# Kernel tuning notes

Measured on AMD Instinct MI355X. Metric: run time of the kernel, lower is better.

The kernel has to match this reference:

```python
import jax, jax.numpy as jnp
import numpy as np

N_HEAD = 4
N_FEAT = 256
D_K = N_FEAT // N_HEAD
MAX_SEQ_LEN = 500
LN_EPS = 1e-6


def setup_inputs() -> dict:
    key = jax.random.key(0)
    ks = jax.random.split(key, 12)
    B, L, F = 64, 500, N_FEAT
    s = lambda fan_in: 1.0 / np.sqrt(fan_in)
    return {
        "q": jax.random.normal(ks[0], (B, L, F), jnp.float32),
        "k": jax.random.normal(ks[1], (B, L, F), jnp.float32),
        "v": jax.random.normal(ks[2], (B, L, F), jnp.float32),
        # weights stored as [in, out] (torch Linear transposed)
        "w_qs": jax.random.normal(ks[3], (F, F), jnp.float32) * s(F),
        "w_vs": jax.random.normal(ks[4], (F, F), jnp.float32) * s(F),
        "w1": jax.random.normal(ks[5], (D_K, D_K), jnp.float32) * s(D_K),
        "b1": jax.random.normal(ks[6], (D_K,), jnp.float32) * s(D_K),
        "w2": jax.random.normal(ks[7], (D_K, MAX_SEQ_LEN), jnp.float32) * s(D_K),
        "b2": jax.random.normal(ks[8], (MAX_SEQ_LEN,), jnp.float32) * s(D_K),
        "fc_w": jax.random.normal(ks[9], (F, F), jnp.float32) * s(F),
        "ln_g": jnp.ones((F,), jnp.float32),
        "ln_b": jnp.zeros((F,), jnp.float32),
    }


def reference(q, k, v, w_qs, w_vs, w1, b1, w2, b2, fc_w, ln_g, ln_b):
    B, L, F = q.shape
    H, dk = N_HEAD, D_K
    residual = q
    # head projections -> [B, H, L, dk]
    qh = (q @ w_qs).reshape(B, L, H, dk).transpose(0, 2, 1, 3)
    vh = (v @ w_vs).reshape(B, L, H, dk).transpose(0, 2, 1, 3)
    # dense synthesizer: relu(q W1 + b1) W2 + b2, slice to len_q
    weight = jax.nn.relu(qh @ w1 + b1)
    attn = (weight @ w2 + b2)[..., :L]            # [B, H, L, L]
    attn = jax.nn.softmax(attn, axis=-1)
    out = attn @ vh                                # [B, H, L, dk]
    out = out.transpose(0, 2, 1, 3).reshape(B, L, F)
    out = out @ fc_w + residual
    # LayerNorm(eps=1e-6)
    mu = jnp.mean(out, axis=-1, keepdims=True)
    var = jnp.var(out, axis=-1, keepdims=True)
    out = (out - mu) * jax.lax.rsqrt(var + LN_EPS) * ln_g + ln_b
    return out
```

## Files before the change

### kernel.cpp

```cpp
#include <hip/hip_runtime.h>
#include <math.h>

#define B_   64
#define L_   500
#define F_   256
#define H_   4
#define DK   64
#define LOG2E 1.44269504088896340736f

typedef unsigned short u16;
typedef unsigned int   u32;
typedef __attribute__((ext_vector_type(8))) short short8;
typedef __attribute__((ext_vector_type(4))) float f32x4;

static __device__ __forceinline__ u16 f2bf(float f) {
    u32 u = __float_as_uint(f);
    u32 r = (u + 0x7FFFu + ((u >> 16) & 1u)) >> 16;
    return (u16)r;
}
static __device__ __forceinline__ u32 pk_bf16_up(float x, float y) {
    u32 xb = __float_as_uint(x) + 0x8000u;
    u32 yb = __float_as_uint(y) + 0x8000u;
    return (xb >> 16) | (yb & 0xFFFF0000u);
}
static __device__ __forceinline__ float exp2_fast(float x) {
#if __has_builtin(__builtin_amdgcn_exp2f)
    return __builtin_amdgcn_exp2f(x);
#else
    return exp2f(x);
#endif
}

typedef __attribute__((address_space(3))) u32 lds32;
typedef const __attribute__((address_space(1))) u32 gbl32;
static __device__ __forceinline__ void gload_lds16(const u16* g, u16* l) {
    __builtin_amdgcn_global_load_lds((gbl32*)g, (lds32*)l, 16, 0, 0);
}

__global__ __launch_bounds__(256) void prep_kernel(
    const float* __restrict__ wq, const float* __restrict__ wv,
    const float* __restrict__ fcw, const float* __restrict__ w1,
    const float* __restrict__ w2, const float* __restrict__ b2,
    u16* __restrict__ wqT, u16* __restrict__ wvT, u16* __restrict__ fcwT,
    u16* __restrict__ w1T, u16* __restrict__ w2sw,
    u16* __restrict__ qh_bf, u16* __restrict__ vhT, float* __restrict__ b2p)
{
    int t = blockIdx.x * 256 + threadIdx.x;
    int stride = gridDim.x * 256;
    for (int i = t; i < 256 * 256; i += stride) {
        int n = i >> 8, k = i & 255;
        wqT[i]  = f2bf(wq[k * 256 + n]);
        wvT[i]  = f2bf(wv[k * 256 + n]);
        fcwT[i] = f2bf(fcw[k * 256 + n]);
    }
    for (int i = t; i < 64 * 64; i += stride) {
        int n = i >> 6, k = i & 63;
        w1T[i] = f2bf(w1[k * 64 + n]);
    }
    for (int i = t; i < 512 * 64; i += stride) {
        int cc  = i >> 12;
        int row = (i >> 6) & 63;
        int kc  = i & 63;
        int n   = cc * 64 + row;
        int kl  = kc ^ ((row & 7) << 3);
        w2sw[i] = f2bf((n < 500 ? w2[kl * 500 + n] : 0.f) * LOG2E);
    }
    for (int i = t; i < 512; i += stride)
        b2p[i] = (i < 500) ? b2[i] * LOG2E : -1e30f;
    for (int i = t; i < 3072; i += stride)
        qh_bf[8192000 + i] = 0;
    for (int i = t; i < 196608; i += stride) {
        int bh = i / 768;
        int r  = i - bh * 768;
        int d  = r / 12;
        int kk = 52 + (r - d * 12);
        vhT[((size_t)((bh * 8 + 7) * 64 + d)) * 64 + (kk ^ ((d & 7) << 3))] = 0;
    }
}

__global__ __launch_bounds__(512) void proj_kernel(
    const float* __restrict__ q, const float* __restrict__ v,
    const u16* __restrict__ wqT, const u16* __restrict__ wvT,
    u16* __restrict__ qh_bf, u16* __restrict__ vhT)
{
    const int which = blockIdx.y;
    const float* __restrict__ x = which ? v : q;
    const u16*   __restrict__ wT = which ? wvT : wqT;

    __shared__ u16 Xs[64][72];
    __shared__ u16 Ws[256][72];

    const int tid  = threadIdx.x;
    const int wvid = tid >> 6, ln = tid & 63;
    const int n16  = ln & 15, quad = ln >> 4;
    const int wr   = wvid >> 2, wc = wvid & 3;
    const int row0 = blockIdx.x * 64;

    f32x4 acc[2][4];
    #pragma unroll
    for (int mt = 0; mt < 2; mt++)
        #pragma unroll
        for (int nt = 0; nt < 4; nt++) acc[mt][nt] = (f32x4){0.f, 0.f, 0.f, 0.f};

    for (int kc = 0; kc < 256; kc += 64) {
        #pragma unroll
        for (int j = 0; j < 2; j++) {
            int idx = tid + 512 * j;
            int m = idx >> 4, k4 = idx & 15;
            float4 a = *(const float4*)&x[(size_t)(row0 + m) * 256 + kc + k4 * 4];
            __align__(8) u16 t4[4] = {f2bf(a.x), f2bf(a.y), f2bf(a.z), f2bf(a.w)};
            *(uint2*)&Xs[m][k4 * 4] = *(const uint2*)t4;
        }
        #pragma unroll
        for (int j = 0; j < 4; j++) {
            int idx = tid + 512 * j;
            int n = idx >> 3, k8 = idx & 7;
            *(uint4*)&Ws[n][k8 * 8] = *(const uint4*)&wT[n * 256 + kc + k8 * 8];
        }
        __syncthreads();
        #pragma unroll
        for (int ks = 0; ks < 2; ks++) {
            short8 af[2], bfr[4];
            #pragma unroll
            for (int mt = 0; mt < 2; mt++)
                af[mt] = *(const short8*)&Xs[wr * 32 + mt * 16 + n16][ks * 32 + quad * 8];
            #pragma unroll
            for (int nt = 0; nt < 4; nt++)
                bfr[nt] = *(const short8*)&Ws[wc * 64 + nt * 16 + n16][ks * 32 + quad * 8];
            #pragma unroll
            for (int mt = 0; mt < 2; mt++)
                #pragma unroll
                for (int nt = 0; nt < 4; nt++)
                    acc[mt][nt] = __builtin_amdgcn_mfma_f32_16x16x32_bf16(
                        af[mt], bfr[nt], acc[mt][nt], 0, 0, 0);
        }
        __syncthreads();
    }

    if (which == 0) {
        #pragma unroll
        for (int mt = 0; mt < 2; mt++) {
            int m0 = row0 + wr * 32 + mt * 16 + quad * 4;
            int b  = m0 / 500;
            int l0 = m0 - 500 * b;
            #pragma unroll
            for (int nt = 0; nt < 4; nt++) {
                int d = nt * 16 + n16;
                u16* dst = qh_bf + ((size_t)((b * 4 + wc) * 500 + l0)) * 64 + d;
                #pragma unroll
                for (int i = 0; i < 4; i++)
                    dst[(size_t)i * 64] = f2bf(acc[mt][nt][i]);
            }
        }
    } else {
        #pragma unroll
        for (int mt = 0; mt < 2; mt++) {
            int m0 = row0 + wr * 32 + mt * 16 + quad * 4;
            int b  = m0 / 500;
            int l0 = m0 - 500 * b;
            int cc = l0 >> 6, kk = l0 & 63;
            #pragma unroll
            for (int nt = 0; nt < 4; nt++) {
                int d = nt * 16 + n16;
                __align__(8) u16 t4[4];
                #pragma unroll
                for (int i = 0; i < 4; i++) t4[i] = f2bf(acc[mt][nt][i]);
                size_t base = ((size_t)(((b * 4 + wc) * 8 + cc) * 64 + d)) * 64;
                *(uint2*)&vhT[base + (kk ^ ((d & 7) << 3))] = *(const uint2*)t4;
            }
        }
    }
}

__global__ __launch_bounds__(512, 1) void attn_kernel(
    const u16* __restrict__ qh, const u16* __restrict__ vhT,
    const u16* __restrict__ w1T, const float* __restrict__ b1,
    const u16* __restrict__ w2sw, const float* __restrict__ b2p,
    u16* __restrict__ ctx)
{
    __shared__ __align__(16) u16 w2all[32768];
    __shared__ __align__(16) u16 v_s[2][4096];
    __shared__ __align__(16) float b2s[512];
    __shared__ __align__(16) u16 scr[8][4][16][72];

    const int tid  = threadIdx.x;
    const int wv   = tid >> 6;
    const int ln   = tid & 63;
    const int n16  = ln & 15;
    const int quad = ln >> 4;
    const int bh   = blockIdx.x;
    const int r0   = wv * 64;

    const u16* vg = vhT + (size_t)bh * 32768;

    {
        int base = wv * 4096;
        #pragma unroll
        for (int j = 0; j < 8; j++)
            gload_lds16(w2sw + base + j * 512 + ln * 8, &w2all[base + j * 512]);
        gload_lds16(vg + wv * 512 + ln * 8, &v_s[0][wv * 512]);
        if (wv < 2)
            gload_lds16((const u16*)b2p + wv * 512 + ln * 8, (u16*)&b2s[wv * 256]);
    }

    const int b = bh >> 2, h = bh & 3;

    {
        short8 a0[4], a1[4];
        #pragma unroll
        for (int rg = 0; rg < 4; rg++) {
            const u16* qbase =
                qh + ((size_t)(bh * 500 + r0 + rg * 16 + n16)) * 64;
            a0[rg] = *(const short8*)(qbase + quad * 8);
            a1[rg] = *(const short8*)(qbase + 32 + quad * 8);
        }
        #pragma unroll
        for (int nt = 0; nt < 4; nt++) {
            const u16* wb = w1T + (nt * 16 + n16) * 64;
            short8 wA0 = *(const short8*)(wb + quad * 8);
            short8 wA1 = *(const short8*)(wb + 32 + quad * 8);
            float4 bv = *(const float4*)&b1[nt * 16 + quad * 4];
            #pragma unroll
            for (int rg = 0; rg < 4; rg++) {
                f32x4 c = {bv.x, bv.y, bv.z, bv.w};
                c = __builtin_amdgcn_mfma_f32_16x16x32_bf16(wA0, a0[rg], c, 0, 0, 0);
                c = __builtin_amdgcn_mfma_f32_16x16x32_bf16(wA1, a1[rg], c, 0, 0, 0);
                u32 p01 = pk_bf16_up(fmaxf(c[0], 0.f), fmaxf(c[1], 0.f));
                u32 p23 = pk_bf16_up(fmaxf(c[2], 0.f), fmaxf(c[3], 0.f));
                *(uint2*)&scr[wv][rg][n16][nt * 16 + quad * 4] =
                    make_uint2(p01, p23);
            }
        }
    }
    short8 sa0[4], sa1[4];
    #pragma unroll
    for (int rg = 0; rg < 4; rg++) {
        sa0[rg] = *(const short8*)&scr[wv][rg][n16][quad * 8];
        sa1[rg] = *(const short8*)&scr[wv][rg][n16][32 + quad * 8];
    }

    f32x4 oacc[4][4];
    #pragma unroll
    for (int rg = 0; rg < 4; rg++)
        #pragma unroll
        for (int nt = 0; nt < 4; nt++)
            oacc[rg][nt] = (f32x4){0.f, 0.f, 0.f, 0.f};
    float sm[4] = {0.f, 0.f, 0.f, 0.f};

    __syncthreads();

    #pragma unroll 2
    for (int cc = 0; cc < 8; cc++) {
        if (cc < 7)
            gload_lds16(vg + (cc + 1) * 4096 + wv * 512 + ln * 8,
                        &v_s[(cc + 1) & 1][wv * 512]);
        const u16* vbuf = &v_s[cc & 1][0];

        #pragma unroll
        for (int t = 0; t < 4; t++) {
            int r  = t * 16 + n16;
            int sw = (r & 7) << 3;
            const u16* wb = &w2all[cc * 4096 + r * 64];
            short8 wA0 = *(const short8*)&wb[(quad * 8) ^ sw];
            short8 wA1 = *(const short8*)&wb[(32 + quad * 8) ^ sw];
            float4 bv = *(const float4*)&b2s[cc * 64 + t * 16 + quad * 4];
            #pragma unroll
            for (int rg = 0; rg < 4; rg++) {
                f32x4 c = {bv.x, bv.y, bv.z, bv.w};
                c = __builtin_amdgcn_mfma_f32_16x16x32_bf16(wA0, sa0[rg], c, 0, 0, 0);
                c = __builtin_amdgcn_mfma_f32_16x16x32_bf16(wA1, sa1[rg], c, 0, 0, 0);
                float e0 = exp2_fast(c[0]);
                float e1 = exp2_fast(c[1]);
                float e2 = exp2_fast(c[2]);
                float e3 = exp2_fast(c[3]);
                sm[rg] += (e0 + e1) + (e2 + e3);
                *(uint2*)&scr[wv][rg][n16][t * 16 + quad * 4] =
                    make_uint2(pk_bf16_up(e0, e1), pk_bf16_up(e2, e3));
            }
        }
        #pragma unroll
        for (int ks = 0; ks < 2; ks++) {
            short8 pa[4];
            #pragma unroll
            for (int rg = 0; rg < 4; rg++)
                pa[rg] = *(const short8*)&scr[wv][rg][n16][ks * 32 + quad * 8];
            #pragma unroll
            for (int nt = 0; nt < 4; nt++) {
                int d   = nt * 16 + n16;
                int swd = (d & 7) << 3;
                short8 vb = *(const short8*)&vbuf[d * 64 +
                                                  ((ks * 32 + quad * 8) ^ swd)];
                #pragma unroll
                for (int rg = 0; rg < 4; rg++)
                    oacc[rg][nt] = __builtin_amdgcn_mfma_f32_16x16x32_bf16(
                        pa[rg], vb, oacc[rg][nt], 0, 0, 0);
            }
        }
        __syncthreads();
    }

    #pragma unroll
    for (int rg = 0; rg < 4; rg++) {
        float smt = sm[rg];
        smt += __shfl_xor(smt, 16);
        smt += __shfl_xor(smt, 32);
        #pragma unroll
        for (int i = 0; i < 4; i++) {
            int lrow = r0 + rg * 16 + quad * 4 + i;
            float si = __shfl(smt, quad * 4 + i);
            if (lrow < 500) {
                float s = 1.f / si;
                u16* dst = &ctx[((size_t)(b * 500 + lrow)) * 256 + h * 64];
                #pragma unroll
                for (int nt = 0; nt < 4; nt++)
                    dst[nt * 16 + n16] = f2bf(oacc[rg][nt][i] * s);
            }
        }
    }
}

__global__ __launch_bounds__(512) void final_kernel(
    const u16* __restrict__ ctx, const u16* __restrict__ fcwT,
    const float* __restrict__ qres, const float* __restrict__ g,
    const float* __restrict__ bta, float* __restrict__ out)
{
    __shared__ u16 Xs[64][72];
    __shared__ u16 Ws[256][72];
    __shared__ float red[4][2][64];
    __shared__ float murs[2][64];

    const int tid  = threadIdx.x;
    const int wvid = tid >> 6, ln = tid & 63;
    const int n16  = ln & 15, quad = ln >> 4;
    const int wr   = wvid >> 2, wc = wvid & 3;
    const int row0 = blockIdx.x * 64;

    f32x4 acc[2][4];
    #pragma unroll
    for (int mt = 0; mt < 2; mt++)
        #pragma unroll
        for (int nt = 0; nt < 4; nt++) acc[mt][nt] = (f32x4){0.f, 0.f, 0.f, 0.f};

    for (int kc = 0; kc < 256; kc += 64) {
        {
            int idx = tid;
            int m = idx >> 3, k8 = idx & 7;
            *(uint4*)&Xs[m][k8 * 8] =
                *(const uint4*)&ctx[(size_t)(row0 + m) * 256 + kc + k8 * 8];
        }
        #pragma unroll
        for (int j = 0; j < 4; j++) {
            int idx = tid + 512 * j;
            int n = idx >> 3, k8 = idx & 7;
            *(uint4*)&Ws[n][k8 * 8] = *(const uint4*)&fcwT[n * 256 + kc + k8 * 8];
        }
        __syncthreads();
        #pragma unroll
        for (int ks = 0; ks < 2; ks++) {
            short8 af[2], bfr[4];
            #pragma unroll
            for (int mt = 0; mt < 2; mt++)
                af[mt] = *(const short8*)&Xs[wr * 32 + mt * 16 + n16][ks * 32 + quad * 8];
            #pragma unroll
            for (int nt = 0; nt < 4; nt++)
                bfr[nt] = *(const short8*)&Ws[wc * 64 + nt * 16 + n16][ks * 32 + quad * 8];
            #pragma unroll
            for (int mt = 0; mt < 2; mt++)
                #pragma unroll
                for (int nt = 0; nt < 4; nt++)
                    acc[mt][nt] = __builtin_amdgcn_mfma_f32_16x16x32_bf16(
                        af[mt], bfr[nt], acc[mt][nt], 0, 0, 0);
        }
        __syncthreads();
    }

    #pragma unroll
    for (int mt = 0; mt < 2; mt++) {
        int m0 = row0 + wr * 32 + mt * 16 + quad * 4;
        #pragma unroll
        for (int i = 0; i < 4; i++) {
            const float* rp = &qres[(size_t)(m0 + i) * 256 + wc * 64 + n16];
            #pragma unroll
            for (int nt = 0; nt < 4; nt++)
                acc[mt][nt][i] += rp[nt * 16];
        }
    }
    #pragma unroll
    for (int mt = 0; mt < 2; mt++) {
        #pragma unroll
        for (int i = 0; i < 4; i++) {
            float s1 = 0.f, s2 = 0.f;
            #pragma unroll
            for (int nt = 0; nt < 4; nt++) {
                float vv = acc[mt][nt][i];
                s1 += vv; s2 += vv * vv;
            }
            #pragma unroll
            for (int off = 1; off < 16; off <<= 1) {
                s1 += __shfl_xor(s1, off);
                s2 += __shfl_xor(s2, off);
            }
            if (n16 == 0) {
                int r = wr * 32 + mt * 16 + quad * 4 + i;
                red[wc][0][r] = s1;
                red[wc][1][r] = s2;
            }
        }
    }
    __syncthreads();
    if (tid < 64) {
        float S1 = red[0][0][tid] + red[1][0][tid] + red[2][0][tid] + red[3][0][tid];
        float S2 = red[0][1][tid] + red[1][1][tid] + red[2][1][tid] + red[3][1][tid];
        float mu  = S1 * 0.00390625f;
        float var = S2 * 0.00390625f - mu * mu;
        murs[0][tid] = mu;
        murs[1][tid] = rsqrtf(var + 1e-6f);
    }
    __syncthreads();

    float gv[4], bv[4];
    #pragma unroll
    for (int nt = 0; nt < 4; nt++) {
        int col = wc * 64 + nt * 16 + n16;
        gv[nt] = g[col];
        bv[nt] = bta[col];
    }
    #pragma unroll
    for (int mt = 0; mt < 2; mt++) {
        int rb = wr * 32 + mt * 16 + quad * 4;
        #pragma unroll
        for (int i = 0; i < 4; i++) {
            float mu = murs[0][rb + i];
            float rs = murs[1][rb + i];
            float* op = &out[(size_t)(row0 + rb + i) * 256 + wc * 64 + n16];
            #pragma unroll
            for (int nt = 0; nt < 4; nt++)
                op[nt * 16] = (acc[mt][nt][i] - mu) * rs * gv[nt] + bv[nt];
        }
    }
}

extern "C" void kernel_launch(void* const* d_in, const int* in_sizes, int n_in,
                              void* d_out, int out_size, void* d_ws, size_t ws_size,
                              hipStream_t stream)
{
    const float* q   = (const float*)d_in[0];
    const float* v   = (const float*)d_in[2];
    const float* wqs = (const float*)d_in[3];
    const float* wvs = (const float*)d_in[4];
    const float* w1  = (const float*)d_in[5];
    const float* b1  = (const float*)d_in[6];
    const float* w2  = (const float*)d_in[7];
    const float* b2  = (const float*)d_in[8];
    const float* fcw = (const float*)d_in[9];
    const float* lng = (const float*)d_in[10];
    const float* lnb = (const float*)d_in[11];
    float* out = (float*)d_out;

    u16* qh_bf = (u16*)d_ws;
    u16* vhT   = qh_bf + 8200192;
    u16* w1T   = vhT + 8388608;
    u16* w2sw  = w1T + 4096;
    u16* wqT   = w2sw + 32768;
    u16* wvT   = wqT + 65536;
    u16* fcwT  = wvT + 65536;
    u16* ctx   = fcwT + 65536;
    float* b2p = (float*)(qh_bf + 8195072);

    prep_kernel <<<dim3(64),     256, 0, stream>>>(wqs, wvs, fcw, w1, w2, b2,
                                                   wqT, wvT, fcwT, w1T, w2sw,
                                                   qh_bf, vhT, b2p);
    proj_kernel <<<dim3(500, 2), 512, 0, stream>>>(q, v, wqT, wvT, qh_bf, vhT);
    attn_kernel <<<dim3(256),    512, 0, stream>>>(qh_bf, vhT, w1T, b1, w2sw, b2p, ctx);
    final_kernel<<<dim3(500),    512, 0, stream>>>(ctx, fcwT, q, lng, lnb, out);
}
```

Baseline: 83.58 us.

## Restructure projection GEMM with 128-row tiles, swizzled LDS and async double-buffered weights

After: 89.60 us. +7.2%, slower.

```diff
diff --git a/kernel.cpp b/kernel.cpp
--- a/kernel.cpp
+++ b/kernel.cpp
@@ -41,7 +41,7 @@
     const float* __restrict__ wq, const float* __restrict__ wv,
     const float* __restrict__ fcw, const float* __restrict__ w1,
     const float* __restrict__ w2, const float* __restrict__ b2,
-    u16* __restrict__ wqT, u16* __restrict__ wvT, u16* __restrict__ fcwT,
+    u16* __restrict__ wqsw, u16* __restrict__ wvsw, u16* __restrict__ fcwT,
     u16* __restrict__ w1T, u16* __restrict__ w2sw,
     u16* __restrict__ qh_bf, u16* __restrict__ vhT, float* __restrict__ b2p)
 {
@@ -49,9 +49,15 @@
     int stride = gridDim.x * 256;
     for (int i = t; i < 256 * 256; i += stride) {
         int n = i >> 8, k = i & 255;
-        wqT[i]  = f2bf(wq[k * 256 + n]);
-        wvT[i]  = f2bf(wv[k * 256 + n]);
         fcwT[i] = f2bf(fcw[k * 256 + n]);
+    }
+    for (int i = t; i < 256 * 256; i += stride) {
+        int kc = i >> 14;
+        int n  = (i >> 6) & 255;
+        int k  = i & 63;
+        int kl = kc * 64 + (k ^ ((n & 7) << 3));
+        wqsw[i] = f2bf(wq[kl * 256 + n]);
+        wvsw[i] = f2bf(wv[kl * 256 + n]);
     }
     for (int i = t; i < 64 * 64; i += stride) {
         int n = i >> 6, k = i & 63;
@@ -78,57 +84,78 @@
     }
 }
 
-__global__ __launch_bounds__(512) void proj_kernel(
+__global__ __launch_bounds__(512, 1) void proj_kernel(
     const float* __restrict__ q, const float* __restrict__ v,
-    const u16* __restrict__ wqT, const u16* __restrict__ wvT,
+    const u16* __restrict__ wqsw, const u16* __restrict__ wvsw,
     u16* __restrict__ qh_bf, u16* __restrict__ vhT)
 {
     const int which = blockIdx.y;
     const float* __restrict__ x = which ? v : q;
-    const u16*   __restrict__ wT = which ? wvT : wqT;
-
-    __shared__ u16 Xs[64][72];
-    __shared__ u16 Ws[256][72];
+    const u16*   __restrict__ wsw = which ? wvsw : wqsw;
+
+    __shared__ __align__(16) u16 Xs[128 * 256];
+    __shared__ __align__(16) u16 Ws[2][16384];
 
     const int tid  = threadIdx.x;
     const int wvid = tid >> 6, ln = tid & 63;
     const int n16  = ln & 15, quad = ln >> 4;
     const int wr   = wvid >> 2, wc = wvid & 3;
-    const int row0 = blockIdx.x * 64;
-
-    f32x4 acc[2][4];
-    #pragma unroll
-    for (int mt = 0; mt < 2; mt++)
+    const int row0 = blockIdx.x * 128;
+
+    float4 xv[16];
+    #pragma unroll
+    for (int j = 0; j < 16; j++) {
+        int idx = tid + 512 * j;
+        int m = idx >> 6, k4 = idx & 63;
+        xv[j] = *(const float4*)&x[(size_t)(row0 + m) * 256 + k4 * 4];
+    }
+    #pragma unroll
+    for (int j = 0; j < 4; j++)
+        gload_lds16(wsw + wvid * 2048 + j * 512 + ln * 8,
+                    &Ws[0][wvid * 2048 + j * 512]);
+    #pragma unroll
+    for (int j = 0; j < 16; j++) {
+        int idx = tid + 512 * j;
+        int m = idx >> 6, k = (idx & 63) * 4;
+        int kx = k ^ ((m & 7) << 3);
+        *(uint2*)&Xs[m * 256 + kx] =
+            make_uint2(pk_bf16_up(xv[j].x, xv[j].y), pk_bf16_up(xv[j].z, xv[j].w));
+    }
+
+    f32x4 acc[4][4];
+    #pragma unroll
+    for (int mt = 0; mt < 4; mt++)
         #pragma unroll
         for (int nt = 0; nt < 4; nt++) acc[mt][nt] = (f32x4){0.f, 0.f, 0.f, 0.f};
 
-    for (int kc = 0; kc < 256; kc += 64) {
-        #pragma unroll
-        for (int j = 0; j < 2; j++) {
-            int idx = tid + 512 * j;
-            int m = idx >> 4, k4 = idx & 15;
-            float4 a = *(const float4*)&x[(size_t)(row0 + m) * 256 + kc + k4 * 4];
-            __align__(8) u16 t4[4] = {f2bf(a.x), f2bf(a.y), f2bf(a.z), f2bf(a.w)};
-            *(uint2*)&Xs[m][k4 * 4] = *(const uint2*)t4;
-        }
-        #pragma unroll
-        for (int j = 0; j < 4; j++) {
-            int idx = tid + 512 * j;
-            int n = idx >> 3, k8 = idx & 7;
-            *(uint4*)&Ws[n][k8 * 8] = *(const uint4*)&wT[n * 256 + kc + k8 * 8];
-        }
-        __syncthreads();
+    __syncthreads();
+
+    #pragma unroll 2
+    for (int cc = 0; cc < 4; cc++) {
+        if (cc < 3) {
+            #pragma unroll
+            for (int j = 0; j < 4; j++)
+                gload_lds16(wsw + (cc + 1) * 16384 + wvid * 2048 + j * 512 + ln * 8,
+                            &Ws[(cc + 1) & 1][wvid * 2048 + j * 512]);
+        }
+        const u16* wb = &Ws[cc & 1][0];
         #pragma unroll
         for (int ks = 0; ks < 2; ks++) {
-            short8 af[2], bfr[4];
-            #pragma unroll
-            for (int mt = 0; mt < 2; mt++)
-                af[mt] = *(const short8*)&Xs[wr * 32 + mt * 16 + n16][ks * 32 + quad * 8];
-            #pragma unroll
-            for (int nt = 0; nt < 4; nt++)
-                bfr[nt] = *(const short8*)&Ws[wc * 64 + nt * 16 + n16][ks * 32 + quad * 8];
-            #pragma unroll
-            for (int mt = 0; mt < 2; mt++)
+            short8 af[4], bfr[4];
+            #pragma unroll
+            for (int mt = 0; mt < 4; mt++) {
+                int m = wr * 64 + mt * 16 + n16;
+                int k = cc * 64 + ks * 32 + quad * 8;
+                af[mt] = *(const short8*)&Xs[m * 256 + (k ^ ((m & 7) << 3))];
+            }
+            #pragma unroll
+            for (int nt = 0; nt < 4; nt++) {
+                int r = wc * 64 + nt * 16 + n16;
+                bfr[nt] = *(const short8*)&wb[r * 64 +
+                                              ((ks * 32 + quad * 8) ^ ((r & 7) << 3))];
+            }
+            #pragma unroll
+            for (int mt = 0; mt < 4; mt++)
                 #pragma unroll
                 for (int nt = 0; nt < 4; nt++)
                     acc[mt][nt] = __builtin_amdgcn_mfma_f32_16x16x32_bf16(
@@ -139,8 +166,8 @@
 
     if (which == 0) {
         #pragma unroll
-        for (int mt = 0; mt < 2; mt++) {
-            int m0 = row0 + wr * 32 + mt * 16 + quad * 4;
+        for (int mt = 0; mt < 4; mt++) {
+            int m0 = row0 + wr * 64 + mt * 16 + quad * 4;
             int b  = m0 / 500;
             int l0 = m0 - 500 * b;
             #pragma unroll
@@ -154,18 +181,18 @@
         }
     } else {
         #pragma unroll
-        for (int mt = 0; mt < 2; mt++) {
-            int m0 = row0 + wr * 32 + mt * 16 + quad * 4;
+        for (int mt = 0; mt < 4; mt++) {
+            int m0 = row0 + wr * 64 + mt * 16 + quad * 4;
             int b  = m0 / 500;
             int l0 = m0 - 500 * b;
-            int cc = l0 >> 6, kk = l0 & 63;
+            int vc = l0 >> 6, kk = l0 & 63;
             #pragma unroll
             for (int nt = 0; nt < 4; nt++) {
                 int d = nt * 16 + n16;
                 __align__(8) u16 t4[4];
                 #pragma unroll
                 for (int i = 0; i < 4; i++) t4[i] = f2bf(acc[mt][nt][i]);
-                size_t base = ((size_t)(((b * 4 + wc) * 8 + cc) * 64 + d)) * 64;
+                size_t base = ((size_t)(((b * 4 + wc) * 8 + vc) * 64 + d)) * 64;
                 *(uint2*)&vhT[base + (kk ^ ((d & 7) << 3))] = *(const uint2*)t4;
             }
         }
@@ -461,16 +488,16 @@
     u16* vhT   = qh_bf + 8200192;
     u16* w1T   = vhT + 8388608;
     u16* w2sw  = w1T + 4096;
-    u16* wqT   = w2sw + 32768;
-    u16* wvT   = wqT + 65536;
-    u16* fcwT  = wvT + 65536;
+    u16* wqsw  = w2sw + 32768;
+    u16* wvsw  = wqsw + 65536;
+    u16* fcwT  = wvsw + 65536;
     u16* ctx   = fcwT + 65536;
     float* b2p = (float*)(qh_bf + 8195072);
 
     prep_kernel <<<dim3(64),     256, 0, stream>>>(wqs, wvs, fcw, w1, w2, b2,
-                                                   wqT, wvT, fcwT, w1T, w2sw,
+                                                   wqsw, wvsw, fcwT, w1T, w2sw,
                                                    qh_bf, vhT, b2p);
-    proj_kernel <<<dim3(500, 2), 512, 0, stream>>>(q, v, wqT, wvT, qh_bf, vhT);
+    proj_kernel <<<dim3(250, 2), 512, 0, stream>>>(q, v, wqsw, wvsw, qh_bf, vhT);
     attn_kernel <<<dim3(256),    512, 0, stream>>>(qh_bf, vhT, w1T, b1, w2sw, b2p, ctx);
     final_kernel<<<dim3(500),    512, 0, stream>>>(ctx, fcwT, q, lng, lnb, out);
 }
```

## Pre-swizzle projection weights into MFMA fragment order and double-buffer input tile

Applied to the files above, without the earlier changes.

New measurement: 85.24 us. No clear change (+2.0%).

```diff
diff --git a/kernel.cpp b/kernel.cpp
--- a/kernel.cpp
+++ b/kernel.cpp
@@ -41,7 +41,7 @@
     const float* __restrict__ wq, const float* __restrict__ wv,
     const float* __restrict__ fcw, const float* __restrict__ w1,
     const float* __restrict__ w2, const float* __restrict__ b2,
-    u16* __restrict__ wqT, u16* __restrict__ wvT, u16* __restrict__ fcwT,
+    u16* __restrict__ wqf, u16* __restrict__ wvf, u16* __restrict__ fcwT,
     u16* __restrict__ w1T, u16* __restrict__ w2sw,
     u16* __restrict__ qh_bf, u16* __restrict__ vhT, float* __restrict__ b2p)
 {
@@ -49,9 +49,18 @@
     int stride = gridDim.x * 256;
     for (int i = t; i < 256 * 256; i += stride) {
         int n = i >> 8, k = i & 255;
-        wqT[i]  = f2bf(wq[k * 256 + n]);
-        wvT[i]  = f2bf(wv[k * 256 + n]);
         fcwT[i] = f2bf(fcw[k * 256 + n]);
+    }
+    for (int i = t; i < 65536; i += stride) {
+        int j  = i & 7;
+        int ln = (i >> 3) & 63;
+        int tn = (i >> 9) & 15;
+        int ks = (i >> 13) & 1;
+        int kc = i >> 14;
+        int k  = kc * 64 + ks * 32 + (ln >> 4) * 8 + j;
+        int n  = tn * 16 + (ln & 15);
+        wqf[i] = f2bf(wq[k * 256 + n]);
+        wvf[i] = f2bf(wv[k * 256 + n]);
     }
     for (int i = t; i < 64 * 64; i += stride) {
         int n = i >> 6, k = i & 63;
@@ -80,15 +89,14 @@
 
 __global__ __launch_bounds__(512) void proj_kernel(
     const float* __restrict__ q, const float* __restrict__ v,
-    const u16* __restrict__ wqT, const u16* __restrict__ wvT,
+    const u16* __restrict__ wqf, const u16* __restrict__ wvf,
     u16* __restrict__ qh_bf, u16* __restrict__ vhT)
 {
     const int which = blockIdx.y;
     const float* __restrict__ x = which ? v : q;
-    const u16*   __restrict__ wT = which ? wvT : wqT;
-
-    __shared__ u16 Xs[64][72];
-    __shared__ u16 Ws[256][72];
+    const u16*   __restrict__ wf = which ? wvf : wqf;
+
+    __shared__ __align__(16) u16 Xs[2][64][72];
 
     const int tid  = threadIdx.x;
     const int wvid = tid >> 6, ln = tid & 63;
@@ -102,37 +110,47 @@
         #pragma unroll
         for (int nt = 0; nt < 4; nt++) acc[mt][nt] = (f32x4){0.f, 0.f, 0.f, 0.f};
 
-    for (int kc = 0; kc < 256; kc += 64) {
-        #pragma unroll
-        for (int j = 0; j < 2; j++) {
-            int idx = tid + 512 * j;
-            int m = idx >> 4, k4 = idx & 15;
-            float4 a = *(const float4*)&x[(size_t)(row0 + m) * 256 + kc + k4 * 4];
-            __align__(8) u16 t4[4] = {f2bf(a.x), f2bf(a.y), f2bf(a.z), f2bf(a.w)};
-            *(uint2*)&Xs[m][k4 * 4] = *(const uint2*)t4;
-        }
-        #pragma unroll
-        for (int j = 0; j < 4; j++) {
-            int idx = tid + 512 * j;
-            int n = idx >> 3, k8 = idx & 7;
-            *(uint4*)&Ws[n][k8 * 8] = *(const uint4*)&wT[n * 256 + kc + k8 * 8];
-        }
-        __syncthreads();
+    #pragma unroll
+    for (int j = 0; j < 2; j++) {
+        int idx = tid + 512 * j;
+        int m = idx >> 4, k4 = idx & 15;
+        float4 a = *(const float4*)&x[(size_t)(row0 + m) * 256 + k4 * 4];
+        *(uint2*)&Xs[0][m][k4 * 4] =
+            make_uint2(pk_bf16_up(a.x, a.y), pk_bf16_up(a.z, a.w));
+    }
+    __syncthreads();
+
+    #pragma unroll
+    for (int kc = 0; kc < 4; kc++) {
+        const int cur = kc & 1;
+        if (kc < 3) {
+            #pragma unroll
+            for (int j = 0; j < 2; j++) {
+                int idx = tid + 512 * j;
+                int m = idx >> 4, k4 = idx & 15;
+                float4 a = *(const float4*)&x[(size_t)(row0 + m) * 256 +
+                                              (kc + 1) * 64 + k4 * 4];
+                *(uint2*)&Xs[cur ^ 1][m][k4 * 4] =
+                    make_uint2(pk_bf16_up(a.x, a.y), pk_bf16_up(a.z, a.w));
+            }
+        }
         #pragma unroll
         for (int ks = 0; ks < 2; ks++) {
-            short8 af[2], bfr[4];
+            short8 af[2];
             #pragma unroll
             for (int mt = 0; mt < 2; mt++)
-                af[mt] = *(const short8*)&Xs[wr * 32 + mt * 16 + n16][ks * 32 + quad * 8];
-            #pragma unroll
-            for (int nt = 0; nt < 4; nt++)
-                bfr[nt] = *(const short8*)&Ws[wc * 64 + nt * 16 + n16][ks * 32 + quad * 8];
-            #pragma unroll
-            for (int mt = 0; mt < 2; mt++)
-                #pragma unroll
-                for (int nt = 0; nt < 4; nt++)
+                af[mt] = *(const short8*)&Xs[cur][wr * 32 + mt * 16 + n16]
+                                            [ks * 32 + quad * 8];
+            #pragma unroll
+            for (int nt = 0; nt < 4; nt++) {
+                const u16* fp = wf + ((((kc * 2 + ks) * 16) + (wc * 4 + nt)) * 64
+                                      + ln) * 8;
+                short8 bfr = *(const short8*)fp;
+                #pragma unroll
+                for (int mt = 0; mt < 2; mt++)
                     acc[mt][nt] = __builtin_amdgcn_mfma_f32_16x16x32_bf16(
-                        af[mt], bfr[nt], acc[mt][nt], 0, 0, 0);
+                        af[mt], bfr, acc[mt][nt], 0, 0, 0);
+            }
         }
         __syncthreads();
     }
@@ -158,15 +176,15 @@
             int m0 = row0 + wr * 32 + mt * 16 + quad * 4;
             int b  = m0 / 500;
             int l0 = m0 - 500 * b;
-            int cc = l0 >> 6, kk = l0 & 63;
+            int vc = l0 >> 6, kk2 = l0 & 63;
             #pragma unroll
             for (int nt = 0; nt < 4; nt++) {
                 int d = nt * 16 + n16;
                 __align__(8) u16 t4[4];
                 #pragma unroll
                 for (int i = 0; i < 4; i++) t4[i] = f2bf(acc[mt][nt][i]);
-                size_t base = ((size_t)(((b * 4 + wc) * 8 + cc) * 64 + d)) * 64;
-                *(uint2*)&vhT[base + (kk ^ ((d & 7) << 3))] = *(const uint2*)t4;
+                size_t base = ((size_t)(((b * 4 + wc) * 8 + vc) * 64 + d)) * 64;
+                *(uint2*)&vhT[base + (kk2 ^ ((d & 7) << 3))] = *(const uint2*)t4;
             }
         }
     }
@@ -461,16 +479,16 @@
     u16* vhT   = qh_bf + 8200192;
     u16* w1T   = vhT + 8388608;
     u16* w2sw  = w1T + 4096;
-    u16* wqT   = w2sw + 32768;
-    u16* wvT   = wqT + 65536;
-    u16* fcwT  = wvT + 65536;
+    u16* wqf   = w2sw + 32768;
+    u16* wvf   = wqf + 65536;
+    u16* fcwT  = wvf + 65536;
     u16* ctx   = fcwT + 65536;
     float* b2p = (float*)(qh_bf + 8195072);
 
     prep_kernel <<<dim3(64),     256, 0, stream>>>(wqs, wvs, fcw, w1, w2, b2,
-                                                   wqT, wvT, fcwT, w1T, w2sw,
+                                                   wqf, wvf, fcwT, w1T, w2sw,
                                                    qh_bf, vhT, b2p);
-    proj_kernel <<<dim3(500, 2), 512, 0, stream>>>(q, v, wqT, wvT, qh_bf, vhT);
+    proj_kernel <<<dim3(500, 2), 512, 0, stream>>>(q, v, wqf, wvf, qh_bf, vhT);
     attn_kernel <<<dim3(256),    512, 0, stream>>>(qh_bf, vhT, w1T, b1, w2sw, b2p, ctx);
     final_kernel<<<dim3(500),    512, 0, stream>>>(ctx, fcwT, q, lng, lnb, out);
 }
```
